# Kernel optimization log

Measured on AMD Instinct MI355X. Metric: run time of the kernel, lower is better.

The kernel has to match this reference:

```python
import jax, jax.numpy as jnp
import numpy as np

N_NODES = 40000
N_EDGES = 640000
D_IN, D_HID, D_OUT = 128, 128, 40


def _gcn_layer(x, src, dst, norm, W, b, n):
    # PyG GCNConv: h = x @ W; aggregate norm * h[src] at dst; add bias.
    h = x @ W
    msg = norm[:, None] * h[src]          # [E+N, d] gathered messages
    return jax.ops.segment_sum(msg, dst, num_segments=n) + b


def setup_inputs() -> dict:
    key = jax.random.key(0)
    ks = jax.random.split(key, 8)
    x = jax.random.normal(ks[0], (N_NODES, D_IN), dtype=jnp.float32)
    edge_index = jax.random.randint(ks[1], (2, N_EDGES), 0, N_NODES)
    s_in = 1.0 / np.sqrt(D_IN)
    s_hid = 1.0 / np.sqrt(D_HID)
    W1 = jax.random.normal(ks[2], (D_IN, D_HID), dtype=jnp.float32) * s_in
    b1 = jnp.zeros((D_HID,), dtype=jnp.float32)
    W2 = jax.random.normal(ks[3], (D_HID, D_HID), dtype=jnp.float32) * s_hid
    b2 = jnp.zeros((D_HID,), dtype=jnp.float32)
    W3 = jax.random.normal(ks[4], (D_HID, D_OUT), dtype=jnp.float32) * s_hid
    b3 = jnp.zeros((D_OUT,), dtype=jnp.float32)
    return {"x": x, "edge_index": edge_index, "W1": W1, "b1": b1,
            "W2": W2, "b2": b2, "W3": W3, "b3": b3}


def reference(x, edge_index, W1, b1, W2, b2, W3, b3):
    n = x.shape[0]
    src = edge_index[0].astype(jnp.int32)
    dst = edge_index[1].astype(jnp.int32)

    # --- GCN normalization with self-loops (PyG GCNConv defaults) ---
    loops = jnp.arange(n, dtype=jnp.int32)
    src2 = jnp.concatenate([src, loops])
    dst2 = jnp.concatenate([dst, loops])
    deg = jax.ops.segment_sum(jnp.ones_like(dst2, dtype=x.dtype), dst2,
                              num_segments=n)
    dis = jnp.where(deg > 0, jax.lax.rsqrt(deg), 0.0)
    norm = dis[src2] * dis[dst2]          # [E+N]

    h = jax.nn.relu(_gcn_layer(x, src2, dst2, norm, W1, b1, n))
    h = jax.nn.relu(_gcn_layer(h, src2, dst2, norm, W2, b2, n))
    out = _gcn_layer(h, src2, dst2, norm, W3, b3, n)

    # --- reg_loss = trace(A @ A), A = dense COO adjacency (dupes summed) ---
    # trace(A@A) = sum_{i,j} A[i,j] * A[j,i]
    #            = sum over edge instances (i,j) of multiplicity of (j,i).
    # Computed sparsely via sorted key lookup instead of NxN densification.
    keys = src * n + dst                  # unique int32 key per (i,j)
    skeys = jnp.sort(keys)
    rev = dst * n + src
    lo = jnp.searchsorted(skeys, rev, side="left")
    hi = jnp.searchsorted(skeys, rev, side="right")
    reg_loss = jnp.sum((hi - lo).astype(jnp.float32))

    return jax.nn.log_softmax(out, axis=1), reg_loss
```

## Files before the change

### kernel.cpp

```cpp
#include <hip/hip_runtime.h>
#include <hip/hip_bf16.h>
#include <math.h>

#define NN 40000
#define EE 640000
#define CAP 64
#define MPAD 40064
#define LDS_STRIDE 136
#define FP8_STRIDE 144
#define E4B 625

typedef short bf16x8 __attribute__((ext_vector_type(8)));
typedef float f32x16 __attribute__((ext_vector_type(16)));
typedef float f32x2 __attribute__((ext_vector_type(2)));

__device__ __forceinline__ unsigned bf16rne(float x) {
  unsigned u = __float_as_uint(x);
  return (u + 0x7fffu + ((u >> 16) & 1u)) >> 16;
}
__device__ __forceinline__ unsigned packbf2(float lo, float hi) {
  return bf16rne(lo) | (bf16rne(hi) << 16);
}
__device__ __forceinline__ float dis_of(const int* cnt, int i) {
  return rsqrtf((float)(cnt[i] + 1));
}
__device__ __forceinline__ f32x2 cvt2lo(unsigned u) {
  return __builtin_amdgcn_cvt_pk_f32_fp8((int)u, false);
}
__device__ __forceinline__ f32x2 cvt2hi(unsigned u) {
  return __builtin_amdgcn_cvt_pk_f32_fp8((int)u, true);
}
__device__ __forceinline__ unsigned char f32_to_fp8(float x) {
  return (unsigned char)(__builtin_amdgcn_cvt_pk_fp8_f32(x, x, 0, false) & 0xff);
}

__global__ __launch_bounds__(256) void edge_w_kernel(
    const int4* __restrict__ src4, const int4* __restrict__ dst4,
    int* __restrict__ cnt, unsigned short* __restrict__ csr,
    const float* __restrict__ W1, const float* __restrict__ W2,
    const float* __restrict__ W3, unsigned short* __restrict__ Wt1,
    unsigned short* __restrict__ Wt2, unsigned short* __restrict__ W3t,
    unsigned* __restrict__ Xb32, unsigned* __restrict__ H1b32) {
  int blk = blockIdx.x, t = threadIdx.x;
  if (blk < E4B) {
    int e = blk * 256 + t;
    int4 s = src4[e];
    int4 d = dst4[e];
    int p0 = atomicAdd(&cnt[d.x], 1);
    int p1 = atomicAdd(&cnt[d.y], 1);
    int p2 = atomicAdd(&cnt[d.z], 1);
    int p3 = atomicAdd(&cnt[d.w], 1);
    if (p0 < CAP) csr[d.x * CAP + p0] = (unsigned short)s.x;
    if (p1 < CAP) csr[d.y * CAP + p1] = (unsigned short)s.y;
    if (p2 < CAP) csr[d.z * CAP + p2] = (unsigned short)s.z;
    if (p3 < CAP) csr[d.w * CAP + p3] = (unsigned short)s.w;
  } else if (blk < 753) {
    bool is1 = blk < 689;
    int n = (blk - (is1 ? 625 : 689)) * 2 + (t >> 7);
    int k = t & 127;
    const float* W = is1 ? W1 : W2;
    unsigned short* Wt = is1 ? Wt1 : Wt2;
    Wt[n * 128 + k] = (unsigned short)bf16rne(W[k * 128 + n]);
  } else if (blk < 785) {
    int n = (blk - 753) * 2 + (t >> 7);
    int k = t & 127;
    float v = (n < 40) ? W3[k * 40 + n] : 0.f;
    W3t[n * 128 + k] = (unsigned short)bf16rne(v);
  } else {
    if (t < 32) Xb32[(size_t)NN * 32 + t] = 0u;
    else if (t < 64) H1b32[(size_t)NN * 32 + (t - 32)] = 0u;
  }
}

__global__ __launch_bounds__(256) void fill_x_kernel(
    const int* __restrict__ cnt, const float4* __restrict__ X,
    uint2* __restrict__ Xb8v) {
  int i = blockIdx.x * 256 + threadIdx.x;
  float di = dis_of(cnt, i >> 4);
  float4 a = X[i * 2], b = X[i * 2 + 1];
  int lo = __builtin_amdgcn_cvt_pk_fp8_f32(di * a.x, di * a.y, 0, false);
  lo = __builtin_amdgcn_cvt_pk_fp8_f32(di * a.z, di * a.w, lo, true);
  int hi = __builtin_amdgcn_cvt_pk_fp8_f32(di * b.x, di * b.y, 0, false);
  hi = __builtin_amdgcn_cvt_pk_fp8_f32(di * b.z, di * b.w, hi, true);
  uint2 o;
  o.x = (unsigned)lo;
  o.y = (unsigned)hi;
  Xb8v[i] = o;
}

__device__ __forceinline__ void agg128_body8(
    int node, int sub, const unsigned char* __restrict__ Hb,
    const int* __restrict__ cnt, const unsigned short* __restrict__ csr,
    unsigned* __restrict__ outB) {
  float di = dis_of(cnt, node);
  const unsigned char* Hbs = Hb + sub * 16;
  f32x2 a0, a1, a2, a3, a4, a5, a6, a7;
  {
    uint4 v = *(const uint4*)&Hbs[(size_t)node * 128];
    a0 = cvt2lo(v.x);
    a1 = cvt2hi(v.x);
    a2 = cvt2lo(v.y);
    a3 = cvt2hi(v.y);
    a4 = cvt2lo(v.z);
    a5 = cvt2hi(v.z);
    a6 = cvt2lo(v.w);
    a7 = cvt2hi(v.w);
  }
  int cn = cnt[node];
  cn = cn > CAP ? CAP : cn;
  const unsigned short* row = &csr[node * CAP];
  if (cn > 0) {
    uint4 cs = *(const uint4*)row;
    for (int e = 0; e < cn; e += 8) {
      int rem = cn - e;
      int s0 = cs.x & 0xffff, s1 = cs.x >> 16;
      int s2 = cs.y & 0xffff, s3 = cs.y >> 16;
      int s4 = cs.z & 0xffff, s5 = cs.z >> 16;
      int s6 = cs.w & 0xffff, s7 = cs.w >> 16;
      s1 = rem > 1 ? s1 : NN;
      s2 = rem > 2 ? s2 : NN;
      s3 = rem > 3 ? s3 : NN;
      s4 = rem > 4 ? s4 : NN;
      s5 = rem > 5 ? s5 : NN;
      s6 = rem > 6 ? s6 : NN;
      s7 = rem > 7 ? s7 : NN;
      uint4 v0 = *(const uint4*)&Hbs[(size_t)s0 * 128];
      uint4 v1 = *(const uint4*)&Hbs[(size_t)s1 * 128];
      uint4 v2 = *(const uint4*)&Hbs[(size_t)s2 * 128];
      uint4 v3 = *(const uint4*)&Hbs[(size_t)s3 * 128];
      uint4 v4 = *(const uint4*)&Hbs[(size_t)s4 * 128];
      uint4 v5 = *(const uint4*)&Hbs[(size_t)s5 * 128];
      uint4 v6 = *(const uint4*)&Hbs[(size_t)s6 * 128];
      uint4 v7 = *(const uint4*)&Hbs[(size_t)s7 * 128];
      if (e + 8 < cn) cs = *(const uint4*)&row[e + 8];
#define ACC8(vv)                                    \
  a0 += cvt2lo(vv.x); a1 += cvt2hi(vv.x);           \
  a2 += cvt2lo(vv.y); a3 += cvt2hi(vv.y);           \
  a4 += cvt2lo(vv.z); a5 += cvt2hi(vv.z);           \
  a6 += cvt2lo(vv.w); a7 += cvt2hi(vv.w);
      ACC8(v0);
      ACC8(v1);
      ACC8(v2);
      ACC8(v3);
      ACC8(v4);
      ACC8(v5);
      ACC8(v6);
      ACC8(v7);
#undef ACC8
    }
  }
  unsigned o0 = packbf2(di * a0.x, di * a0.y);
  unsigned o1 = packbf2(di * a1.x, di * a1.y);
  unsigned o2 = packbf2(di * a2.x, di * a2.y);
  unsigned o3 = packbf2(di * a3.x, di * a3.y);
  unsigned o4 = packbf2(di * a4.x, di * a4.y);
  unsigned o5 = packbf2(di * a5.x, di * a5.y);
  unsigned o6 = packbf2(di * a6.x, di * a6.y);
  unsigned o7 = packbf2(di * a7.x, di * a7.y);
  *(uint4*)&outB[(size_t)node * 64 + sub * 8] = make_uint4(o0, o1, o2, o3);
  *(uint4*)&outB[(size_t)node * 64 + sub * 8 + 4] = make_uint4(o4, o5, o6, o7);
}

__global__ __launch_bounds__(256) void agg_reg(
    const unsigned char* __restrict__ Hb8, const int* __restrict__ cnt,
    const unsigned short* __restrict__ csr, unsigned* __restrict__ outB,
    const int* __restrict__ src, const int* __restrict__ dst, int ebase,
    float* __restrict__ out_scalar) {
  int blk = blockIdx.x, t = threadIdx.x;
  if ((blk & 1) == 0) {
    int node = (blk >> 1) * 32 + (t >> 3);
    agg128_body8(node, t & 7, Hb8, cnt, csr, outB);
    return;
  }
  int e = ebase + (blk >> 1) * 256 + t;
  int c = 0;
  {
    int i = src[e];
    unsigned j = (unsigned)dst[e];
    int cn = cnt[i];
    cn = cn > CAP ? CAP : cn;
    const uint4* base = (const uint4*)&csr[i * CAP];
    int full = cn >> 3;
    for (int q = 0; q < full; q++) {
      uint4 v = base[q];
      c += ((v.x & 0xffffu) == j) + ((v.x >> 16) == j);
      c += ((v.y & 0xffffu) == j) + ((v.y >> 16) == j);
      c += ((v.z & 0xffffu) == j) + ((v.z >> 16) == j);
      c += ((v.w & 0xffffu) == j) + ((v.w >> 16) == j);
    }
    int rem = cn & 7;
    if (rem) {
      uint4 v = base[full];
      c += (int)((v.x & 0xffffu) == j);
      c += ((v.x >> 16) == j) & (rem > 1);
      c += ((v.y & 0xffffu) == j) & (rem > 2);
      c += ((v.y >> 16) == j) & (rem > 3);
      c += ((v.z & 0xffffu) == j) & (rem > 4);
      c += ((v.z >> 16) == j) & (rem > 5);
      c += ((v.w & 0xffffu) == j) & (rem > 6);
    }
  }
  float v = (float)c;
  for (int off = 32; off; off >>= 1) v += __shfl_down(v, off, 64);
  __shared__ float ws[4];
  int lane = threadIdx.x & 63, w = threadIdx.x >> 6;
  if (lane == 0) ws[w] = v;
  __syncthreads();
  if (threadIdx.x == 0) atomicAdd(out_scalar, ws[0] + ws[1] + ws[2] + ws[3]);
}

__global__ __launch_bounds__(256) void gemm_mfma(
    const unsigned* __restrict__ Ab, const unsigned* __restrict__ Wt,
    const float* __restrict__ bias, const int* __restrict__ cnt,
    unsigned char* __restrict__ outB8) {
  __shared__ unsigned short At[128 * LDS_STRIDE];
  __shared__ unsigned short Bt[128 * LDS_STRIDE];
  __shared__ float dsh[128];
  int t = threadIdx.x;
  int rowBase = blockIdx.x * 128;
  if (t < 128) {
    int rr = rowBase + t;
    dsh[t] = (rr < NN) ? dis_of(cnt, rr) : 0.f;
  }
  {
    const uint4* ga = (const uint4*)(Ab + (size_t)rowBase * 64);
    const uint4* gw = (const uint4*)Wt;
#pragma unroll
    for (int i = 0; i < 8; i++) {
      int idx = i * 256 + t;
      int r = idx >> 4, c = idx & 15;
      uint4 va = ga[idx];
      uint4 vw = gw[idx];
      *(uint4*)&At[r * LDS_STRIDE + c * 8] = va;
      *(uint4*)&Bt[r * LDS_STRIDE + c * 8] = vw;
    }
  }
  __syncthreads();
  int lane = t & 63, w = t >> 6;
  int m31 = lane & 31;
  int khalf = (lane >> 5) * 8;
  f32x16 acc[4] = {};
#pragma unroll
  for (int ks = 0; ks < 8; ks++) {
    bf16x8 a = *(bf16x8*)&At[(w * 32 + m31) * LDS_STRIDE + ks * 16 + khalf];
#pragma unroll
    for (int nt = 0; nt < 4; nt++) {
      bf16x8 b = *(bf16x8*)&Bt[(nt * 32 + m31) * LDS_STRIDE + ks * 16 + khalf];
      acc[nt] = __builtin_amdgcn_mfma_f32_32x32x16_bf16(a, b, acc[nt], 0, 0, 0);
    }
  }
  __syncthreads();
  unsigned char* Ac = (unsigned char*)At;
  int rsel = (lane >> 5) * 4;
#pragma unroll
  for (int nt = 0; nt < 4; nt++) {
    int col = nt * 32 + m31;
    float bv = bias[col];
#pragma unroll
    for (int r = 0; r < 16; r++) {
      int rl = w * 32 + (r & 3) + 8 * (r >> 2) + rsel;
      float x = fmaxf(acc[nt][r] + bv, 0.f);
      Ac[rl * FP8_STRIDE + col] = f32_to_fp8(dsh[rl] * x);
    }
  }
  __syncthreads();
  {
#pragma unroll
    for (int i = 0; i < 4; i++) {
      int idx = i * 256 + t;
      int r = idx >> 3, c = idx & 7;
      int grow = rowBase + r;
      if (grow < NN) {
        uint4 vv = *(const uint4*)&Ac[r * FP8_STRIDE + c * 16];
        *(uint4*)&outB8[(size_t)grow * 128 + c * 16] = vv;
      }
    }
  }
}

__global__ __launch_bounds__(256) void gemm_mfma2(
    const unsigned* __restrict__ Ab, const unsigned* __restrict__ Wt,
    const float* __restrict__ bias, const int* __restrict__ cnt,
    const unsigned short* __restrict__ W3t, float* __restrict__ G3) {
  __shared__ unsigned short At[128 * LDS_STRIDE];
  __shared__ unsigned short Bt[128 * LDS_STRIDE];
  __shared__ float dsh[128];
  int t = threadIdx.x;
  int rowBase = blockIdx.x * 128;
  if (blockIdx.x == 0 && t < 40) G3[(size_t)NN * 40 + t] = 0.f;
  if (t < 128) {
    int rr = rowBase + t;
    dsh[t] = (rr < NN) ? dis_of(cnt, rr) : 0.f;
  }
  {
    const uint4* ga = (const uint4*)(Ab + (size_t)rowBase * 64);
    const uint4* gw = (const uint4*)Wt;
#pragma unroll
    for (int i = 0; i < 8; i++) {
      int idx = i * 256 + t;
      int r = idx >> 4, c = idx & 15;
      uint4 va = ga[idx];
      uint4 vw = gw[idx];
      *(uint4*)&At[r * LDS_STRIDE + c * 8] = va;
      *(uint4*)&Bt[r * LDS_STRIDE + c * 8] = vw;
    }
  }
  __syncthreads();
  int lane = t & 63, w = t >> 6;
  int m31 = lane & 31;
  int khalf = (lane >> 5) * 8;
  f32x16 acc[4] = {};
#pragma unroll
  for (int ks = 0; ks < 8; ks++) {
    bf16x8 a = *(bf16x8*)&At[(w * 32 + m31) * LDS_STRIDE + ks * 16 + khalf];
#pragma unroll
    for (int nt = 0; nt < 4; nt++) {
      bf16x8 b = *(bf16x8*)&Bt[(nt * 32 + m31) * LDS_STRIDE + ks * 16 + khalf];
      acc[nt] = __builtin_amdgcn_mfma_f32_32x32x16_bf16(a, b, acc[nt], 0, 0, 0);
    }
  }
  __syncthreads();
  int rsel = (lane >> 5) * 4;
#pragma unroll
  for (int nt = 0; nt < 4; nt++) {
    int col = nt * 32 + m31;
    float bv = bias[col];
#pragma unroll
    for (int r = 0; r < 16; r++) {
      int rl = w * 32 + (r & 3) + 8 * (r >> 2) + rsel;
      float x = fmaxf(acc[nt][r] + bv, 0.f);
      At[rl * LDS_STRIDE + col] = (unsigned short)bf16rne(dsh[rl] * x);
    }
  }
  {
    const uint4* gw3 = (const uint4*)W3t;
#pragma unroll
    for (int i = 0; i < 4; i++) {
      int idx = i * 256 + t;
      int r = idx >> 4, c = idx & 15;
      *(uint4*)&Bt[r * LDS_STRIDE + c * 8] = gw3[idx];
    }
  }
  __syncthreads();
  f32x16 acc2[2] = {};
#pragma unroll
  for (int ks = 0; ks < 8; ks++) {
    bf16x8 a = *(bf16x8*)&At[(w * 32 + m31) * LDS_STRIDE + ks * 16 + khalf];
#pragma unroll
    for (int nt = 0; nt < 2; nt++) {
      bf16x8 b = *(bf16x8*)&Bt[(nt * 32 + m31) * LDS_STRIDE + ks * 16 + khalf];
      acc2[nt] = __builtin_amdgcn_mfma_f32_32x32x16_bf16(a, b, acc2[nt], 0, 0, 0);
    }
  }
  __syncthreads();
  float* Gst = (float*)At;
#pragma unroll
  for (int nt = 0; nt < 2; nt++) {
    int col = nt * 32 + m31;
    if (col < 40) {
#pragma unroll
      for (int r = 0; r < 16; r++) {
        int rl = w * 32 + (r & 3) + 8 * (r >> 2) + rsel;
        Gst[rl * 40 + col] = acc2[nt][r];
      }
    }
  }
  __syncthreads();
  {
    int lim = NN - rowBase;
    int lim4 = (lim >= 128) ? 1280 : lim * 10;
#pragma unroll
    for (int i = 0; i < 5; i++) {
      int idx = i * 256 + t;
      if (idx < lim4) {
        float4 vv = *(const float4*)&Gst[idx * 4];
        *(float4*)&G3[(size_t)rowBase * 40 + idx * 4] = vv;
      }
    }
  }
}

__global__ __launch_bounds__(256) void agg40_softmax(
    const float* __restrict__ G, const int* __restrict__ cnt,
    const unsigned short* __restrict__ csr, const float* __restrict__ b3,
    float* __restrict__ outp) {
  int node = __builtin_amdgcn_readfirstlane(blockIdx.x * 4 + (threadIdx.x >> 6));
  int lane = threadIdx.x & 63;
  int cl = lane < 40 ? lane : 39;
  float di = dis_of(cnt, node);
  float a = G[(size_t)node * 40 + cl];
  int cn = cnt[node];
  cn = cn > CAP ? CAP : cn;
  const unsigned short* row = &csr[node * CAP];
  if (cn > 0) {
    uint4 cs = *(const uint4*)row;
    for (int e = 0; e < cn; e += 8) {
      int rem = cn - e;
      int s0 = cs.x & 0xffff, s1 = cs.x >> 16;
      int s2 = cs.y & 0xffff, s3 = cs.y >> 16;
      int s4 = cs.z & 0xffff, s5 = cs.z >> 16;
      int s6 = cs.w & 0xffff, s7 = cs.w >> 16;
      s1 = rem > 1 ? s1 : NN;
      s2 = rem > 2 ? s2 : NN;
      s3 = rem > 3 ? s3 : NN;
      s4 = rem > 4 ? s4 : NN;
      s5 = rem > 5 ? s5 : NN;
      s6 = rem > 6 ? s6 : NN;
      s7 = rem > 7 ? s7 : NN;
      float g0 = G[(size_t)s0 * 40 + cl];
      float g1 = G[(size_t)s1 * 40 + cl];
      float g2 = G[(size_t)s2 * 40 + cl];
      float g3 = G[(size_t)s3 * 40 + cl];
      float g4 = G[(size_t)s4 * 40 + cl];
      float g5 = G[(size_t)s5 * 40 + cl];
      float g6 = G[(size_t)s6 * 40 + cl];
      float g7 = G[(size_t)s7 * 40 + cl];
      if (e + 8 < cn) cs = *(const uint4*)&row[e + 8];
      a += g0 + g1 + g2 + g3 + g4 + g5 + g6 + g7;
    }
  }
  float o = di * a + b3[cl];
  float m = (lane < 40) ? o : -1e30f;
  for (int off = 32; off; off >>= 1) m = fmaxf(m, __shfl_xor(m, off, 64));
  float ex = (lane < 40) ? expf(o - m) : 0.f;
  float ssum = ex;
  for (int off = 32; off; off >>= 1) ssum += __shfl_xor(ssum, off, 64);
  float res = o - m - logf(ssum);
  if (lane < 40) outp[(size_t)node * 40 + lane] = res;
}

extern "C" void kernel_launch(void* const* d_in, const int* in_sizes, int n_in,
                              void* d_out, int out_size, void* d_ws,
                              size_t ws_size, hipStream_t stream) {
  const float* X = (const float*)d_in[0];
  const int* ei = (const int*)d_in[1];
  const float* W1 = (const float*)d_in[2];
  const float* b1 = (const float*)d_in[3];
  const float* W2 = (const float*)d_in[4];
  const float* b2 = (const float*)d_in[5];
  const float* W3 = (const float*)d_in[6];
  const float* b3 = (const float*)d_in[7];
  float* out = (float*)d_out;

  const int* src = ei;
  const int* dst = ei + EE;

  char* w = (char*)d_ws;
  auto carve = [&](size_t bytes) {
    char* p = w;
    w += (bytes + 255) & ~(size_t)255;
    return p;
  };
  int* cnt = (int*)carve(NN * 4);
  unsigned short* csr = (unsigned short*)carve((size_t)NN * CAP * 2);
  unsigned short* Wt1 = (unsigned short*)carve(128 * 128 * 2);
  unsigned short* Wt2 = (unsigned short*)carve(128 * 128 * 2);
  unsigned short* W3t = (unsigned short*)carve(64 * 128 * 2);
  unsigned* Ab = (unsigned*)carve((size_t)MPAD * 128 * 2);
  char* blk = carve(((size_t)NN + 1) * 40 * 4 + ((size_t)NN + 1) * 128 * 2);
  unsigned char* Xb8 = (unsigned char*)blk;
  unsigned char* H1b8 = (unsigned char*)blk + ((size_t)NN + 1) * 128;
  float* G3 = (float*)blk;

  (void)hipMemsetAsync(cnt, 0, NN * 4, stream);
  (void)hipMemsetAsync((char*)d_out + (size_t)NN * 40 * 4, 0, 4, stream);

  const int GB = MPAD / 128;

  edge_w_kernel<<<786, 256, 0, stream>>>((const int4*)src, (const int4*)dst,
                                         cnt, csr, W1, W2, W3, Wt1, Wt2, W3t,
                                         (unsigned*)Xb8, (unsigned*)H1b8);
  fill_x_kernel<<<2500, 256, 0, stream>>>(cnt, (const float4*)X, (uint2*)Xb8);
  agg_reg<<<2500, 256, 0, stream>>>(Xb8, cnt, csr, Ab, src, dst, 0,
                                    out + (size_t)NN * 40);
  gemm_mfma<<<GB, 256, 0, stream>>>(Ab, (const unsigned*)Wt1, b1, cnt, H1b8);
  agg_reg<<<2500, 256, 0, stream>>>(H1b8, cnt, csr, Ab, src, dst, EE / 2,
                                    out + (size_t)NN * 40);
  gemm_mfma2<<<GB, 256, 0, stream>>>(Ab, (const unsigned*)Wt2, b2, cnt, W3t,
                                     G3);
  agg40_softmax<<<NN / 4, 256, 0, stream>>>(G3, cnt, csr, b3, out);
}
```

Measured before the change: 204.4 us.

## Store layer-3 features as padded bf16 rows and aggregate eight columns per thread

The final GEMM now writes its 40-wide output as bf16 into 128-byte padded rows (64 columns) instead of fp32 40-wide rows. The last aggregation and log-softmax kernel then assigns 8 threads per node, each loading 16 bytes per neighbor and summing 8 columns, rather than one 64-lane wave per node reading scalar floats. This halves the gathered bytes and issues wider loads with far fewer waves, at the cost of bf16 rounding of the layer-3 features.

```diff
diff --git a/kernel.cpp b/kernel.cpp
--- a/kernel.cpp
+++ b/kernel.cpp
@@ -8,6 +8,7 @@
 #define MPAD 40064
 #define LDS_STRIDE 136
 #define FP8_STRIDE 144
+#define G_STRIDE 72
 #define E4B 625
 
 typedef short bf16x8 __attribute__((ext_vector_type(8)));
@@ -20,6 +21,12 @@
 }
 __device__ __forceinline__ unsigned packbf2(float lo, float hi) {
   return bf16rne(lo) | (bf16rne(hi) << 16);
+}
+__device__ __forceinline__ float bflo(unsigned u) {
+  return __uint_as_float(u << 16);
+}
+__device__ __forceinline__ float bfhi(unsigned u) {
+  return __uint_as_float(u & 0xffff0000u);
 }
 __device__ __forceinline__ float dis_of(const int* cnt, int i) {
   return rsqrtf((float)(cnt[i] + 1));
@@ -281,13 +288,14 @@
 __global__ __launch_bounds__(256) void gemm_mfma2(
     const unsigned* __restrict__ Ab, const unsigned* __restrict__ Wt,
     const float* __restrict__ bias, const int* __restrict__ cnt,
-    const unsigned short* __restrict__ W3t, float* __restrict__ G3) {
+    const unsigned short* __restrict__ W3t, unsigned char* __restrict__ G3b) {
   __shared__ unsigned short At[128 * LDS_STRIDE];
   __shared__ unsigned short Bt[128 * LDS_STRIDE];
   __shared__ float dsh[128];
   int t = threadIdx.x;
   int rowBase = blockIdx.x * 128;
-  if (blockIdx.x == 0 && t < 40) G3[(size_t)NN * 40 + t] = 0.f;
+  if (blockIdx.x == 0 && t < 32)
+    ((unsigned*)G3b)[(size_t)NN * 32 + t] = 0u;
   if (t < 128) {
     int rr = rowBase + t;
     dsh[t] = (rr < NN) ? dis_of(cnt, rr) : 0.f;
@@ -353,42 +361,48 @@
     }
   }
   __syncthreads();
-  float* Gst = (float*)At;
+  unsigned short* Gs = At;
 #pragma unroll
   for (int nt = 0; nt < 2; nt++) {
     int col = nt * 32 + m31;
-    if (col < 40) {
-#pragma unroll
-      for (int r = 0; r < 16; r++) {
-        int rl = w * 32 + (r & 3) + 8 * (r >> 2) + rsel;
-        Gst[rl * 40 + col] = acc2[nt][r];
+#pragma unroll
+    for (int r = 0; r < 16; r++) {
+      int rl = w * 32 + (r & 3) + 8 * (r >> 2) + rsel;
+      Gs[rl * G_STRIDE + col] = (unsigned short)bf16rne(acc2[nt][r]);
+    }
+  }
+  __syncthreads();
+  {
+#pragma unroll
+    for (int i = 0; i < 4; i++) {
+      int idx = i * 256 + t;
+      int r = idx >> 3, c = idx & 7;
+      int grow = rowBase + r;
+      if (grow < NN) {
+        uint4 vv = *(const uint4*)&Gs[r * G_STRIDE + c * 8];
+        *(uint4*)&G3b[(size_t)grow * 128 + c * 16] = vv;
       }
     }
   }
-  __syncthreads();
-  {
-    int lim = NN - rowBase;
-    int lim4 = (lim >= 128) ? 1280 : lim * 10;
-#pragma unroll
-    for (int i = 0; i < 5; i++) {
-      int idx = i * 256 + t;
-      if (idx < lim4) {
-        float4 vv = *(const float4*)&Gst[idx * 4];
-        *(float4*)&G3[(size_t)rowBase * 40 + idx * 4] = vv;
-      }
-    }
-  }
-}
-
-__global__ __launch_bounds__(256) void agg40_softmax(
-    const float* __restrict__ G, const int* __restrict__ cnt,
+}
+
+__global__ __launch_bounds__(256) void agg40b_softmax(
+    const unsigned char* __restrict__ Gb, const int* __restrict__ cnt,
     const unsigned short* __restrict__ csr, const float* __restrict__ b3,
     float* __restrict__ outp) {
-  int node = __builtin_amdgcn_readfirstlane(blockIdx.x * 4 + (threadIdx.x >> 6));
-  int lane = threadIdx.x & 63;
-  int cl = lane < 40 ? lane : 39;
+  int t = threadIdx.x;
+  int node = blockIdx.x * 32 + (t >> 3);
+  int sub = t & 7;
+  const unsigned char* Gs = Gb + sub * 16;
   float di = dis_of(cnt, node);
-  float a = G[(size_t)node * 40 + cl];
+  float a0, a1, a2, a3, a4, a5, a6, a7;
+  {
+    uint4 v = *(const uint4*)&Gs[(size_t)node * 128];
+    a0 = bflo(v.x); a1 = bfhi(v.x);
+    a2 = bflo(v.y); a3 = bfhi(v.y);
+    a4 = bflo(v.z); a5 = bfhi(v.z);
+    a6 = bflo(v.w); a7 = bfhi(v.w);
+  }
   int cn = cnt[node];
   cn = cn > CAP ? CAP : cn;
   const unsigned short* row = &csr[node * CAP];
@@ -407,26 +421,60 @@
       s5 = rem > 5 ? s5 : NN;
       s6 = rem > 6 ? s6 : NN;
       s7 = rem > 7 ? s7 : NN;
-      float g0 = G[(size_t)s0 * 40 + cl];
-      float g1 = G[(size_t)s1 * 40 + cl];
-      float g2 = G[(size_t)s2 * 40 + cl];
-      float g3 = G[(size_t)s3 * 40 + cl];
-      float g4 = G[(size_t)s4 * 40 + cl];
-      float g5 = G[(size_t)s5 * 40 + cl];
-      float g6 = G[(size_t)s6 * 40 + cl];
-      float g7 = G[(size_t)s7 * 40 + cl];
+      uint4 v0 = *(const uint4*)&Gs[(size_t)s0 * 128];
+      uint4 v1 = *(const uint4*)&Gs[(size_t)s1 * 128];
+      uint4 v2 = *(const uint4*)&Gs[(size_t)s2 * 128];
+      uint4 v3 = *(const uint4*)&Gs[(size_t)s3 * 128];
+      uint4 v4 = *(const uint4*)&Gs[(size_t)s4 * 128];
+      uint4 v5 = *(const uint4*)&Gs[(size_t)s5 * 128];
+      uint4 v6 = *(const uint4*)&Gs[(size_t)s6 * 128];
+      uint4 v7 = *(const uint4*)&Gs[(size_t)s7 * 128];
       if (e + 8 < cn) cs = *(const uint4*)&row[e + 8];
-      a += g0 + g1 + g2 + g3 + g4 + g5 + g6 + g7;
-    }
-  }
-  float o = di * a + b3[cl];
-  float m = (lane < 40) ? o : -1e30f;
-  for (int off = 32; off; off >>= 1) m = fmaxf(m, __shfl_xor(m, off, 64));
-  float ex = (lane < 40) ? expf(o - m) : 0.f;
-  float ssum = ex;
-  for (int off = 32; off; off >>= 1) ssum += __shfl_xor(ssum, off, 64);
-  float res = o - m - logf(ssum);
-  if (lane < 40) outp[(size_t)node * 40 + lane] = res;
+#define ACCB(vv)                                    \
+  a0 += bflo(vv.x); a1 += bfhi(vv.x);               \
+  a2 += bflo(vv.y); a3 += bfhi(vv.y);               \
+  a4 += bflo(vv.z); a5 += bfhi(vv.z);               \
+  a6 += bflo(vv.w); a7 += bfhi(vv.w);
+      ACCB(v0);
+      ACCB(v1);
+      ACCB(v2);
+      ACCB(v3);
+      ACCB(v4);
+      ACCB(v5);
+      ACCB(v6);
+      ACCB(v7);
+#undef ACCB
+    }
+  }
+  bool act = sub < 5;
+  int sb = act ? sub : 0;
+  const float4* b34 = (const float4*)b3;
+  float4 bl = b34[sb * 2], bh = b34[sb * 2 + 1];
+  float o0 = di * a0 + bl.x, o1 = di * a1 + bl.y;
+  float o2 = di * a2 + bl.z, o3 = di * a3 + bl.w;
+  float o4 = di * a4 + bh.x, o5 = di * a5 + bh.y;
+  float o6 = di * a6 + bh.z, o7 = di * a7 + bh.w;
+  float m = fmaxf(fmaxf(fmaxf(o0, o1), fmaxf(o2, o3)),
+                  fmaxf(fmaxf(o4, o5), fmaxf(o6, o7)));
+  m = act ? m : -1e30f;
+  m = fmaxf(m, __shfl_xor(m, 1, 64));
+  m = fmaxf(m, __shfl_xor(m, 2, 64));
+  m = fmaxf(m, __shfl_xor(m, 4, 64));
+  float s = expf(o0 - m) + expf(o1 - m) + expf(o2 - m) + expf(o3 - m) +
+            expf(o4 - m) + expf(o5 - m) + expf(o6 - m) + expf(o7 - m);
+  s = act ? s : 0.f;
+  s += __shfl_xor(s, 1, 64);
+  s += __shfl_xor(s, 2, 64);
+  s += __shfl_xor(s, 4, 64);
+  float l = m + logf(s);
+  if (act) {
+    float4 r0, r1;
+    r0.x = o0 - l; r0.y = o1 - l; r0.z = o2 - l; r0.w = o3 - l;
+    r1.x = o4 - l; r1.y = o5 - l; r1.z = o6 - l; r1.w = o7 - l;
+    float* op = &outp[(size_t)node * 40 + sub * 8];
+    *(float4*)op = r0;
+    *(float4*)(op + 4) = r1;
+  }
 }
 
 extern "C" void kernel_launch(void* const* d_in, const int* in_sizes, int n_in,
@@ -457,10 +505,10 @@
   unsigned short* Wt2 = (unsigned short*)carve(128 * 128 * 2);
   unsigned short* W3t = (unsigned short*)carve(64 * 128 * 2);
   unsigned* Ab = (unsigned*)carve((size_t)MPAD * 128 * 2);
-  char* blk = carve(((size_t)NN + 1) * 40 * 4 + ((size_t)NN + 1) * 128 * 2);
+  char* blk = carve(((size_t)NN + 1) * 128 * 2);
   unsigned char* Xb8 = (unsigned char*)blk;
   unsigned char* H1b8 = (unsigned char*)blk + ((size_t)NN + 1) * 128;
-  float* G3 = (float*)blk;
+  unsigned char* G3b = (unsigned char*)blk;
 
   (void)hipMemsetAsync(cnt, 0, NN * 4, stream);
   (void)hipMemsetAsync((char*)d_out + (size_t)NN * 40 * 4, 0, 4, stream);
@@ -477,6 +525,6 @@
   agg_reg<<<2500, 256, 0, stream>>>(H1b8, cnt, csr, Ab, src, dst, EE / 2,
                                     out + (size_t)NN * 40);
   gemm_mfma2<<<GB, 256, 0, stream>>>(Ab, (const unsigned*)Wt2, b2, cnt, W3t,
-                                     G3);
-  agg40_softmax<<<NN / 4, 256, 0, stream>>>(G3, cnt, csr, b3, out);
-}
+                                     G3b);
+  agg40b_softmax<<<1250, 256, 0, stream>>>(G3b, cnt, csr, b3, out);
+}
```

Measured after the change: 194.3 us. -4.9%, faster.
